# Kernel tuning notes

Hardware: AMD Instinct MI355X
Metric: run time of the kernel (lower is better)

The kernel has to match this reference:

```python
import jax, jax.numpy as jnp
import numpy as np
import math

N = 100000      # nodes
E = 1600000     # edges
D = 128         # embedding_size
H = 8           # num_heads
Dh = D // H     # head dim
F = 4 * D       # ffn hidden


def _layer_norm(x, g, b, eps=1e-5):
    mu = jnp.mean(x, axis=-1, keepdims=True)
    var = jnp.mean((x - mu) ** 2, axis=-1, keepdims=True)
    return (x - mu) * jax.lax.rsqrt(var + eps) * g + b


def setup_inputs() -> dict:
    key = jax.random.key(0)
    ks = jax.random.split(key, 12)
    s = 1.0 / math.sqrt(D)
    sf = 1.0 / math.sqrt(F)
    return {
        "feat": jax.random.normal(ks[0], (N, D), dtype=jnp.float32),
        "src": jax.random.randint(ks[1], (E,), 0, N, dtype=jnp.int32),
        "dst": jax.random.randint(ks[2], (E,), 0, N, dtype=jnp.int32),
        "Wq": jax.random.normal(ks[3], (D, D), dtype=jnp.float32) * s,
        "bq": jnp.zeros((D,), jnp.float32),
        "Wk": jax.random.normal(ks[4], (D, D), dtype=jnp.float32) * s,
        "bk": jnp.zeros((D,), jnp.float32),
        "Wv": jax.random.normal(ks[5], (D, D), dtype=jnp.float32) * s,
        "bv": jnp.zeros((D,), jnp.float32),
        "ln_g": jnp.ones((D,), jnp.float32),
        "ln_b": jnp.zeros((D,), jnp.float32),
        "W1": jax.random.normal(ks[6], (D, F), dtype=jnp.float32) * s,
        "b1": jnp.zeros((F,), jnp.float32),
        "alpha": jnp.full((F,), 0.25, jnp.float32),   # PReLU per-channel
        "W2": jax.random.normal(ks[7], (F, D), dtype=jnp.float32) * sf,
        "b2": jnp.zeros((D,), jnp.float32),
    }


def reference(feat, src, dst, Wq, bq, Wk, bk, Wv, bv, ln_g, ln_b, W1, b1, alpha, W2, b2):
    feat_c = jax.lax.stop_gradient(feat)  # feat_c = feat.detach()
    q = (feat @ Wq + bq).reshape(N, H, Dh)
    k = (feat_c @ Wk + bk).reshape(N, H, Dh)
    v = (feat_c @ Wv + bv).reshape(N, H, Dh)

    # u_dot_v: score per edge = <k[src], q[dst]> per head, scaled by sqrt(embedding_size)
    e = jnp.einsum('ehd,ehd->eh', k[src], q[dst]) / math.sqrt(D)  # [E, H]

    # edge_softmax over incoming edges of each destination node
    emax = jax.ops.segment_max(e, dst, num_segments=N)            # [N, H]
    ex = jnp.exp(e - emax[dst])                                   # [E, H]
    denom = jax.ops.segment_sum(ex, dst, num_segments=N)          # [N, H]
    a = ex / denom[dst]                                           # [E, H]

    # u_mul_e + sum: weighted scatter-aggregation into dst nodes
    m = v[src] * a[:, :, None]                                    # [E, H, Dh]
    rst = jax.ops.segment_sum(m, dst, num_segments=N)             # [N, H, Dh]
    rst = rst.reshape(N, D) + feat
    rst = _layer_norm(rst, ln_g, ln_b)

    # out_proj: Linear -> PReLU -> Linear (dropouts are identity at p=0)
    h = rst @ W1 + b1
    h = jnp.where(h > 0, h, alpha * h)
    ffn = h @ W2 + b2
    return _layer_norm(rst + ffn, ln_g, ln_b)  # original reuses ln1
```

## Files before the change

kernel.cpp:

```cpp
#include <hip/hip_runtime.h>
#include <hip/hip_bf16.h>

#define D 128
#define H 8
#define DH 16
#define FF 512
#define NBK 512
#define CHUNK 8192

typedef __hip_bfloat16 bf16;
typedef __attribute__((ext_vector_type(8))) short short8v;
typedef __attribute__((ext_vector_type(4))) float f32x4;

#define MFMA16(a, b, c) __builtin_amdgcn_mfma_f32_16x16x32_bf16((a), (b), (c), 0, 0, 0)

__device__ __forceinline__ unsigned short bfbits(float x) {
    bf16 h = __float2bfloat16(x);
    unsigned short s;
    __builtin_memcpy(&s, &h, 2);
    return s;
}

__device__ __forceinline__ void dec8(uint4 u, float* f) {
    f[0] = __uint_as_float(u.x << 16); f[1] = __uint_as_float(u.x & 0xffff0000u);
    f[2] = __uint_as_float(u.y << 16); f[3] = __uint_as_float(u.y & 0xffff0000u);
    f[4] = __uint_as_float(u.z << 16); f[5] = __uint_as_float(u.z & 0xffff0000u);
    f[6] = __uint_as_float(u.w << 16); f[7] = __uint_as_float(u.w & 0xffff0000u);
}

__global__ __launch_bounds__(256) void wsplit_pack(
    const float* __restrict__ W, unsigned short* __restrict__ Th,
    unsigned short* __restrict__ Tl, int K, int logC)
{
    int i = blockIdx.x * 256 + threadIdx.x;
    int total = K << logC;
    if (i >= total) return;
    int k = i >> logC;
    int n = i & ((1 << logC) - 1);
    float x = W[i];
    unsigned short hb = bfbits(x);
    float hf = __uint_as_float((unsigned)hb << 16);
    unsigned short lb = bfbits(x - hf);
    int NT = 1 << (logC - 4);
    int tile = (k >> 5) * NT + (n >> 4);
    int lane = ((k >> 3) & 3) * 16 + (n & 15);
    int idx = tile * 512 + lane * 8 + (k & 7);
    Th[idx] = hb;
    Tl[idx] = lb;
}

#define QXS 136

__global__ __launch_bounds__(256, 2) void qkv_mfma(
    const float* __restrict__ feat,
    const unsigned short* __restrict__ WTh, const unsigned short* __restrict__ WTl,
    const float* __restrict__ bq, const float* __restrict__ bk, const float* __restrict__ bv,
    bf16* __restrict__ q, bf16* __restrict__ k, bf16* __restrict__ v,
    int N)
{
    __shared__ unsigned short Xh[32 * QXS];
    __shared__ unsigned short Xl[32 * QXS];

    const int tid = threadIdx.x;
    const int n0 = blockIdx.x * 32;

    #pragma unroll
    for (int it = 0; it < 4; it++) {
        int idx = tid + it * 256;
        int row = idx >> 5;
        int part = idx & 31;
        float4 f = make_float4(0.f, 0.f, 0.f, 0.f);
        if (n0 + row < N) f = *(const float4*)(feat + (size_t)(n0 + row) * D + part * 4);
        const float xv[4] = {f.x, f.y, f.z, f.w};
        unsigned short hb[4], lb[4];
        #pragma unroll
        for (int j = 0; j < 4; j++) {
            hb[j] = bfbits(xv[j]);
            float hf = __uint_as_float((unsigned)hb[j] << 16);
            lb[j] = bfbits(xv[j] - hf);
        }
        uint2 ph, pl;
        ph.x = (unsigned)hb[0] | ((unsigned)hb[1] << 16);
        ph.y = (unsigned)hb[2] | ((unsigned)hb[3] << 16);
        pl.x = (unsigned)lb[0] | ((unsigned)lb[1] << 16);
        pl.y = (unsigned)lb[2] | ((unsigned)lb[3] << 16);
        *(uint2*)&Xh[row * QXS + part * 4] = ph;
        *(uint2*)&Xl[row * QXS + part * 4] = pl;
    }
    __syncthreads();

    const int w = tid >> 6, l = tid & 63;
    const int lr = l & 15;
    const int lg = l >> 4;

    f32x4 acc[2][6];
    const f32x4 zero4 = {0.f, 0.f, 0.f, 0.f};
    #pragma unroll
    for (int rt = 0; rt < 2; rt++)
        #pragma unroll
        for (int ct = 0; ct < 6; ct++) acc[rt][ct] = zero4;

    auto ldb = [&](int u, short8v* bh3, short8v* bl3) {
        const int ks = u >> 1, cb = (u & 1) * 3;
        #pragma unroll
        for (int j = 0; j < 3; j++) {
            const int g = w * 6 + cb + j;
            const size_t off = (size_t)(g >> 3) * 16384 +
                               (size_t)((ks * 8 + (g & 7)) * 512 + l * 8);
            bh3[j] = *(const short8v*)&WTh[off];
            bl3[j] = *(const short8v*)&WTl[off];
        }
    };

    short8v pbh[3][3], pbl[3][3];
    ldb(0, pbh[0], pbl[0]);
    ldb(1, pbh[1], pbl[1]);
    short8v ah0, ah1, al0, al1;

    #pragma unroll
    for (int u = 0; u < 8; u++) {
        if (u + 2 < 8) ldb(u + 2, pbh[(u + 2) % 3], pbl[(u + 2) % 3]);
        if ((u & 1) == 0) {
            const int k0 = (u >> 1) * 32;
            ah0 = *(const short8v*)&Xh[lr * QXS + k0 + lg * 8];
            ah1 = *(const short8v*)&Xh[(16 + lr) * QXS + k0 + lg * 8];
            al0 = *(const short8v*)&Xl[lr * QXS + k0 + lg * 8];
            al1 = *(const short8v*)&Xl[(16 + lr) * QXS + k0 + lg * 8];
        }
        const int cb = (u & 1) * 3;
        const short8v* bh = pbh[u % 3];
        const short8v* bl = pbl[u % 3];
        #pragma unroll
        for (int j = 0; j < 3; j++) acc[0][cb + j] = MFMA16(ah0, bh[j], acc[0][cb + j]);
        #pragma unroll
        for (int j = 0; j < 3; j++) acc[1][cb + j] = MFMA16(ah1, bh[j], acc[1][cb + j]);
        #pragma unroll
        for (int j = 0; j < 3; j++) acc[0][cb + j] = MFMA16(ah0, bl[j], acc[0][cb + j]);
        #pragma unroll
        for (int j = 0; j < 3; j++) acc[1][cb + j] = MFMA16(ah1, bl[j], acc[1][cb + j]);
        #pragma unroll
        for (int j = 0; j < 3; j++) acc[0][cb + j] = MFMA16(al0, bh[j], acc[0][cb + j]);
        #pragma unroll
        for (int j = 0; j < 3; j++) acc[1][cb + j] = MFMA16(al1, bh[j], acc[1][cb + j]);
    }

    #pragma unroll
    for (int ct = 0; ct < 6; ct++) {
        const int cbase = w * 96 + ct * 16;
        const int which = cbase >> 7;
        const int colin = (cbase & 127) + lr;
        const float* bias = which == 0 ? bq : (which == 1 ? bk : bv);
        bf16* outp       = which == 0 ? q  : (which == 1 ? k  : v);
        const float bb = bias[colin];
        #pragma unroll
        for (int rt = 0; rt < 2; rt++) {
            #pragma unroll
            for (int i = 0; i < 4; i++) {
                int row = n0 + rt * 16 + lg * 4 + i;
                if (row < N)
                    outp[(size_t)row * D + colin] = __float2bfloat16(acc[rt][ct][i] + bb);
            }
        }
    }
}

__global__ __launch_bounds__(256) void bucket_hist(
    const int* __restrict__ dst, int* __restrict__ bcnt, int E)
{
    __shared__ int bh[NBK];
    for (int j = threadIdx.x; j < NBK; j += 256) bh[j] = 0;
    __syncthreads();
    for (int i = blockIdx.x * 256 + threadIdx.x; i < E; i += gridDim.x * 256)
        atomicAdd(&bh[dst[i] >> 8], 1);
    __syncthreads();
    for (int j = threadIdx.x; j < NBK; j += 256)
        if (bh[j]) atomicAdd(&bcnt[j], bh[j]);
}

__global__ __launch_bounds__(256) void bucket_scan(
    const int* __restrict__ bcnt, int* __restrict__ bofsb, int* __restrict__ gcur)
{
    __shared__ int sA[NBK], sB[NBK];
    const int t = threadIdx.x;
    for (int j = t; j < NBK; j += 256) sA[j] = bcnt[j];
    __syncthreads();
    bool pb = false;
    for (int off = 1; off < NBK; off <<= 1) {
        const int* in = pb ? sB : sA;
        int* o        = pb ? sA : sB;
        for (int j = t; j < NBK; j += 256)
            o[j] = in[j] + (j >= off ? in[j - off] : 0);
        __syncthreads();
        pb = !pb;
    }
    const int* inc = pb ? sB : sA;
    for (int j = t; j < NBK; j += 256) {
        int ex = inc[j] - bcnt[j];
        bofsb[j] = ex;
        gcur[j]  = ex;
    }
}

__global__ __launch_bounds__(256) void binA(
    const int* __restrict__ src, const int* __restrict__ dst,
    int* __restrict__ gcur, unsigned* __restrict__ bpack, int E)
{
    __shared__ int hist[NBK], runc[NBK], gof[NBK];
    const int t = threadIdx.x;
    const int e0 = blockIdx.x * CHUNK;
    const int cnt = min(CHUNK, E - e0);

    for (int j = t; j < NBK; j += 256) { hist[j] = 0; runc[j] = 0; }
    __syncthreads();

    for (int i = t; i < cnt; i += 256)
        atomicAdd(&hist[dst[e0 + i] >> 8], 1);
    __syncthreads();

    for (int j = t; j < NBK; j += 256)
        if (hist[j] > 0) gof[j] = atomicAdd(&gcur[j], hist[j]);
    __syncthreads();

    for (int i = t; i < cnt; i += 256) {
        int d = dst[e0 + i];
        int s = src[e0 + i];
        int b = d >> 8;
        int r = atomicAdd(&runc[b], 1);
        bpack[gof[b] + r] = ((unsigned)(d & 255) << 24) | (unsigned)s;
    }
}

__global__ __launch_bounds__(256) void deg_binned(
    const unsigned* __restrict__ bpack, const int* __restrict__ bofsb,
    const int* __restrict__ bcnt, int* __restrict__ deg, int N)
{
    __shared__ int dc[256];
    const int t = threadIdx.x;
    const int b = blockIdx.x;
    dc[t] = 0;
    __syncthreads();
    const int bstart = bofsb[b], cnt = bcnt[b];
    for (int i = t; i < cnt; i += 256)
        atomicAdd(&dc[bpack[bstart + i] >> 24], 1);
    __syncthreads();
    const int node = b * 256 + t;
    if (node < N) deg[node] = dc[t];
}

__global__ __launch_bounds__(256) void binB(
    const unsigned* __restrict__ bpack, const int* __restrict__ bofsb,
    const int* __restrict__ bcnt, const int* __restrict__ row_off,
    int* __restrict__ csr, int N)
{
    __shared__ int curl[256];
    const int t = threadIdx.x;
    const int b = blockIdx.x;
    const int base = b * 256;
    curl[t] = (base + t < N) ? row_off[base + t] : 0;
    __syncthreads();
    const int bstart = bofsb[b], cnt = bcnt[b];
    for (int i = t; i < cnt; i += 256) {
        unsigned p = bpack[bstart + i];
        int pos = atomicAdd(&curl[p >> 24], 1);
        csr[pos] = (int)(p & 0xFFFFFFu);
    }
}

__global__ __launch_bounds__(256) void scan_bsum(
    const int* __restrict__ deg, int* __restrict__ bsum, int N)
{
    int base = blockIdx.x * 1024;
    int t = threadIdx.x;
    int s = 0;
    #pragma unroll
    for (int j = 0; j < 4; j++) {
        int i = base + t + 256 * j;
        if (i < N) s += deg[i];
    }
    #pragma unroll
    for (int o = 1; o < 64; o <<= 1) s += __shfl_xor(s, o);
    __shared__ int ws[4];
    if ((t & 63) == 0) ws[t >> 6] = s;
    __syncthreads();
    if (t == 0) bsum[blockIdx.x] = ws[0] + ws[1] + ws[2] + ws[3];
}

__global__ void scan_bofs(const int* __restrict__ bsum, int* __restrict__ bofs, int nb)
{
    if (threadIdx.x == 0) {
        int run = 0;
        for (int i = 0; i < nb; i++) { bofs[i] = run; run += bsum[i]; }
    }
}

__global__ __launch_bounds__(256) void scan_write(
    const int* __restrict__ deg, const int* __restrict__ bofs,
    int* __restrict__ row_off, int N)
{
    int t = threadIdx.x;
    int base = blockIdx.x * 1024 + t * 4;
    int d[4]; int tot = 0;
    #pragma unroll
    for (int j = 0; j < 4; j++) {
        int i = base + j;
        d[j] = (i < N) ? deg[i] : 0;
        tot += d[j];
    }
    int incl = tot;
    int lane = t & 63;
    #pragma unroll
    for (int o = 1; o < 64; o <<= 1) {
        int nv = __shfl_up(incl, o);
        if (lane >= o) incl += nv;
    }
    __shared__ int ws[4];
    if (lane == 63) ws[t >> 6] = incl;
    __syncthreads();
    int w = t >> 6;
    int woff = 0;
    #pragma unroll
    for (int kk = 0; kk < 4; kk++) if (kk < w) woff += ws[kk];
    int run = bofs[blockIdx.x] + woff + incl - tot;
    #pragma unroll
    for (int j = 0; j < 4; j++) {
        int i = base + j;
        if (i < N) row_off[i] = run;
        run += d[j];
    }
}

__global__ __launch_bounds__(64) void node_agg(
    const bf16* __restrict__ kb, const bf16* __restrict__ qb, const bf16* __restrict__ vb,
    const int* __restrict__ csr, const int* __restrict__ row_off, const int* __restrict__ deg,
    const float* __restrict__ feat, const float* __restrict__ g, const float* __restrict__ b,
    bf16* __restrict__ rst_ln, int N)
{
    __shared__ float qs[128];
    const int l = threadIdx.x;
    const int n = blockIdx.x;
    if (n >= N) return;

    unsigned qu = *(const unsigned*)(qb + (size_t)n * D + 2 * l);
    qs[2 * l]     = __uint_as_float(qu << 16);
    qs[2 * l + 1] = __uint_as_float(qu & 0xffff0000u);

    const int rs = row_off[n], dn = deg[n];
    const int el = l >> 3, h = l & 7, ha = l >> 3;

    float m = -3.0e38f, lsum = 0.f, acc0 = 0.f, acc1 = 0.f;

    if (dn > 0) {
        int sn = csr[rs + (el < dn ? el : 0)];
        const uint4* kp0 = (const uint4*)(kb + (size_t)sn * D + h * DH);
        uint4 k0 = kp0[0], k1 = kp0[1];

        for (int base = 0; base < dn; base += 8) {
            int sn_n = 0;
            uint4 kn0, kn1;
            const bool more = base + 8 < dn;
            if (more) {
                int ei = base + 8 + el;
                sn_n = csr[rs + (ei < dn ? ei : 0)];
                const uint4* kpn = (const uint4*)(kb + (size_t)sn_n * D + h * DH);
                kn0 = kpn[0]; kn1 = kpn[1];
            }

            const bool valid = base + el < dn;
            float kf[16];
            dec8(k0, kf); dec8(k1, kf + 8);
            const float* qp = &qs[h * DH];
            float s = 0.f;
            #pragma unroll
            for (int i = 0; i < 16; i++) s += kf[i] * qp[i];
            s *= 0.08838834764831845f;
            if (!valid) s = -3.0e38f;

            float cmax = s;
            cmax = fmaxf(cmax, __shfl_xor(cmax, 8));
            cmax = fmaxf(cmax, __shfl_xor(cmax, 16));
            cmax = fmaxf(cmax, __shfl_xor(cmax, 32));
            float m_new = fmaxf(m, cmax);
            float alphaH = __expf(m - m_new);
            float wgt = __expf(s - m_new);
            float wsum = wgt;
            wsum += __shfl_xor(wsum, 8);
            wsum += __shfl_xor(wsum, 16);
            wsum += __shfl_xor(wsum, 32);
            lsum = lsum * alphaH + wsum;
            m = m_new;

            float alphaA = __shfl(alphaH, ha);

            float na0 = 0.f, na1 = 0.f;
            #pragma unroll
            for (int e = 0; e < 8; e++) {
                int sne = __shfl(sn, e * 8);
                unsigned vu = *(const unsigned*)(vb + (size_t)sne * D + 2 * l);
                float wv = __shfl(wgt, e * 8 + ha);
                na0 += wv * __uint_as_float(vu << 16);
                na1 += wv * __uint_as_float(vu & 0xffff0000u);
            }
            acc0 = acc0 * alphaA + na0;
            acc1 = acc1 * alphaA + na1;

            if (more) { sn = sn_n; k0 = kn0; k1 = kn1; }
        }
    }

    float den = __shfl(lsum, ha);
    float v0 = (den > 0.f) ? acc0 / den : 0.f;
    float v1 = (den > 0.f) ? acc1 / den : 0.f;

    float2 fv = *(const float2*)(feat + (size_t)n * D + 2 * l);
    v0 += fv.x; v1 += fv.y;

    float s1 = v0 + v1, s2 = v0 * v0 + v1 * v1;
    #pragma unroll
    for (int o = 1; o < 64; o <<= 1) {
        s1 += __shfl_xor(s1, o);
        s2 += __shfl_xor(s2, o);
    }
    float mu = s1 * (1.f / 128.f);
    float var = s2 * (1.f / 128.f) - mu * mu;
    float rsq = rsqrtf(var + 1e-5f);
    float y0 = (v0 - mu) * rsq * g[2 * l]     + b[2 * l];
    float y1 = (v1 - mu) * rsq * g[2 * l + 1] + b[2 * l + 1];
    unsigned pk = (unsigned)bfbits(y0) | ((unsigned)bfbits(y1) << 16);
    *(unsigned*)(rst_ln + (size_t)n * D + 2 * l) = pk;
}

#define BM 32
#define XS 136
#define HS 520
#define YS 132

__global__ __launch_bounds__(256, 2) void ffn_mfma(
    const bf16* __restrict__ rst_ln,
    const unsigned short* __restrict__ W1Th, const unsigned short* __restrict__ W1Tl,
    const float* __restrict__ b1, const float* __restrict__ alpha,
    const unsigned short* __restrict__ W2Th, const unsigned short* __restrict__ W2Tl,
    const float* __restrict__ b2,
    const float* __restrict__ g, const float* __restrict__ bln,
    float* __restrict__ out, int N)
{
    __shared__ unsigned short Xs[BM * XS];
    __shared__ unsigned short HhBuf[BM * HS];
    __shared__ unsigned short Hl[BM * HS];

    const int tid = threadIdx.x;
    const int n0 = blockIdx.x * BM;

    #pragma unroll
    for (int it = 0; it < 2; it++) {
        int idx = tid + it * 256;
        int row = idx >> 4;
        int part = idx & 15;
        uint4 u = make_uint4(0u, 0u, 0u, 0u);
        if (n0 + row < N) u = *(const uint4*)(rst_ln + (size_t)(n0 + row) * D + part * 8);
        *(uint4*)&Xs[row * XS + part * 8] = u;
    }
    __syncthreads();

    const int w = tid >> 6, l = tid & 63;
    const int lr = l & 15;
    const int lg = l >> 4;

    const int colbase = w * 128;
    f32x4 acc1[2][8];
    const f32x4 zero4 = {0.f, 0.f, 0.f, 0.f};
    #pragma unroll
    for (int rt = 0; rt < 2; rt++)
        #pragma unroll
        for (int ct = 0; ct < 8; ct++) acc1[rt][ct] = zero4;

    auto ldb1 = [&](int u, short8v* bh4, short8v* bl4) {
        const int ks = u >> 1, cb = (u & 1) * 4;
        #pragma unroll
        for (int j = 0; j < 4; j++) {
            const size_t off = (size_t)((ks * 32 + w * 8 + cb + j) * 512 + l * 8);
            bh4[j] = *(const short8v*)&W1Th[off];
            bl4[j] = *(const short8v*)&W1Tl[off];
        }
    };

    {
        short8v pbh[3][4], pbl[3][4];
        ldb1(0, pbh[0], pbl[0]);
        ldb1(1, pbh[1], pbl[1]);
        short8v a0, a1;
        #pragma unroll
        for (int u = 0; u < 8; u++) {
            if (u + 2 < 8) ldb1(u + 2, pbh[(u + 2) % 3], pbl[(u + 2) % 3]);
            if ((u & 1) == 0) {
                const int k0 = (u >> 1) * 32;
                a0 = *(const short8v*)&Xs[lr * XS + k0 + lg * 8];
                a1 = *(const short8v*)&Xs[(16 + lr) * XS + k0 + lg * 8];
            }
            const int cb = (u & 1) * 4;
            const short8v* bh = pbh[u % 3];
            const short8v* bl = pbl[u % 3];
            #pragma unroll
            for (int j = 0; j < 4; j++) acc1[0][cb + j] = MFMA16(a0, bh[j], acc1[0][cb + j]);
            #pragma unroll
            for (int j = 0; j < 4; j++) acc1[1][cb + j] = MFMA16(a1, bh[j], acc1[1][cb + j]);
            #pragma unroll
            for (int j = 0; j < 4; j++) acc1[0][cb + j] = MFMA16(a0, bl[j], acc1[0][cb + j]);
            #pragma unroll
            for (int j = 0; j < 4; j++) acc1[1][cb + j] = MFMA16(a1, bl[j], acc1[1][cb + j]);
        }
    }

    #pragma unroll
    for (int ct = 0; ct < 8; ct++) {
        const int col = colbase + ct * 16 + lr;
        const float bb = b1[col];
        const float aa = alpha[col];
        #pragma unroll
        for (int rt = 0; rt < 2; rt++) {
            #pragma unroll
            for (int i = 0; i < 4; i++) {
                const int row = rt * 16 + lg * 4 + i;
                float hv = acc1[rt][ct][i] + bb;
                hv = hv > 0.f ? hv : aa * hv;
                unsigned short hb = bfbits(hv);
                float hf = __uint_as_float((unsigned)hb << 16);
                unsigned short lb = bfbits(hv - hf);
                HhBuf[row * HS + col] = hb;
                Hl[row * HS + col]    = lb;
            }
        }
    }
    __syncthreads();

    const int ob = w * 32;
    f32x4 acc2[2][2];
    #pragma unroll
    for (int rt = 0; rt < 2; rt++)
        #pragma unroll
        for (int ct = 0; ct < 2; ct++) acc2[rt][ct] = zero4;

    auto ldb2 = [&](int ks, short8v* bh2, short8v* bl2) {
        #pragma unroll
        for (int ct = 0; ct < 2; ct++) {
            const size_t off = (size_t)((ks * 8 + w * 2 + ct) * 512 + l * 8);
            bh2[ct] = *(const short8v*)&W2Th[off];
            bl2[ct] = *(const short8v*)&W2Tl[off];
        }
    };

    {
        short8v p2h[4][2], p2l[4][2];
        #pragma unroll
        for (int s = 0; s < 3; s++) ldb2(s, p2h[s], p2l[s]);
        #pragma unroll
        for (int ks = 0; ks < 16; ks++) {
            const int slot = ks & 3;
            if (ks + 3 < 16) ldb2(ks + 3, p2h[(ks + 3) & 3], p2l[(ks + 3) & 3]);
            const int k0 = ks * 32;
            short8v ah0 = *(const short8v*)&HhBuf[lr * HS + k0 + lg * 8];
            short8v ah1 = *(const short8v*)&HhBuf[(16 + lr) * HS + k0 + lg * 8];
            short8v al0 = *(const short8v*)&Hl[lr * HS + k0 + lg * 8];
            short8v al1 = *(const short8v*)&Hl[(16 + lr) * HS + k0 + lg * 8];
            const short8v* bh = p2h[slot];
            const short8v* bl = p2l[slot];
            acc2[0][0] = MFMA16(ah0, bh[0], acc2[0][0]);
            acc2[0][1] = MFMA16(ah0, bh[1], acc2[0][1]);
            acc2[1][0] = MFMA16(ah1, bh[0], acc2[1][0]);
            acc2[1][1] = MFMA16(ah1, bh[1], acc2[1][1]);
            acc2[0][0] = MFMA16(ah0, bl[0], acc2[0][0]);
            acc2[0][1] = MFMA16(ah0, bl[1], acc2[0][1]);
            acc2[1][0] = MFMA16(ah1, bl[0], acc2[1][0]);
            acc2[1][1] = MFMA16(ah1, bl[1], acc2[1][1]);
            acc2[0][0] = MFMA16(al0, bh[0], acc2[0][0]);
            acc2[0][1] = MFMA16(al0, bh[1], acc2[0][1]);
            acc2[1][0] = MFMA16(al1, bh[0], acc2[1][0]);
            acc2[1][1] = MFMA16(al1, bh[1], acc2[1][1]);
        }
    }
    __syncthreads();

    float* Yb = (float*)HhBuf;
    #pragma unroll
    for (int ct = 0; ct < 2; ct++) {
        const int col = ob + ct * 16 + lr;
        const float bb = b2[col];
        #pragma unroll
        for (int rt = 0; rt < 2; rt++) {
            #pragma unroll
            for (int i = 0; i < 4; i++) {
                const int row = rt * 16 + lg * 4 + i;
                float xr = __uint_as_float((unsigned)Xs[row * XS + col] << 16);
                Yb[row * YS + col] = acc2[rt][ct][i] + bb + xr;
            }
        }
    }
    __syncthreads();

    {
        const int row = tid >> 3;
        const int sub = tid & 7;
        const int c0 = sub * 16;
        const float* Yr = Yb + row * YS + c0;
        f32x4 v0 = *(const f32x4*)(Yr + 0);
        f32x4 v1 = *(const f32x4*)(Yr + 4);
        f32x4 v2 = *(const f32x4*)(Yr + 8);
        f32x4 v3 = *(const f32x4*)(Yr + 12);
        float s1 = 0.f, s2 = 0.f;
        #pragma unroll
        for (int c = 0; c < 4; c++) {
            s1 += v0[c] + v1[c] + v2[c] + v3[c];
            s2 += v0[c] * v0[c] + v1[c] * v1[c] + v2[c] * v2[c] + v3[c] * v3[c];
        }
        #pragma unroll
        for (int o = 1; o < 8; o <<= 1) {
            s1 += __shfl_xor(s1, o);
            s2 += __shfl_xor(s2, o);
        }
        float mu = s1 * (1.f / 128.f);
        float var = s2 * (1.f / 128.f) - mu * mu;
        float rs = rsqrtf(var + 1e-5f);
        const int gr = n0 + row;
        if (gr < N) {
            float* op = out + (size_t)gr * D + c0;
            f32x4 g0 = *(const f32x4*)(g + c0 + 0),  g1 = *(const f32x4*)(g + c0 + 4);
            f32x4 g2 = *(const f32x4*)(g + c0 + 8),  g3 = *(const f32x4*)(g + c0 + 12);
            f32x4 b0 = *(const f32x4*)(bln + c0 + 0), b1v = *(const f32x4*)(bln + c0 + 4);
            f32x4 b2v = *(const f32x4*)(bln + c0 + 8), b3 = *(const f32x4*)(bln + c0 + 12);
            *(f32x4*)(op + 0)  = (v0 - mu) * rs * g0 + b0;
            *(f32x4*)(op + 4)  = (v1 - mu) * rs * g1 + b1v;
            *(f32x4*)(op + 8)  = (v2 - mu) * rs * g2 + b2v;
            *(f32x4*)(op + 12) = (v3 - mu) * rs * g3 + b3;
        }
    }
}

extern "C" void kernel_launch(void* const* d_in, const int* in_sizes, int n_in,
                              void* d_out, int out_size, void* d_ws, size_t ws_size,
                              hipStream_t stream) {
    const float* feat = (const float*)d_in[0];
    const int*   src  = (const int*)d_in[1];
    const int*   dst  = (const int*)d_in[2];
    const float* Wq   = (const float*)d_in[3];
    const float* bq   = (const float*)d_in[4];
    const float* Wk   = (const float*)d_in[5];
    const float* bk   = (const float*)d_in[6];
    const float* Wv   = (const float*)d_in[7];
    const float* bv   = (const float*)d_in[8];
    const float* ln_g = (const float*)d_in[9];
    const float* ln_b = (const float*)d_in[10];
    const float* W1   = (const float*)d_in[11];
    const float* b1   = (const float*)d_in[12];
    const float* alp  = (const float*)d_in[13];
    const float* W2   = (const float*)d_in[14];
    const float* b2   = (const float*)d_in[15];
    float* out = (float*)d_out;

    const int N = in_sizes[0] / D;
    const int E = in_sizes[1];
    const int nb = (N + 1023) / 1024;
    const int nbk = (N + 255) >> 8;

    char* p = (char*)d_ws;
    auto take = [&](size_t bytes) { char* r = p; p += (bytes + 255) & ~(size_t)255; return r; };
    bf16* qb    = (bf16*)take((size_t)N * D * 2);
    bf16* kb    = (bf16*)take((size_t)N * D * 2);
    bf16* vb    = (bf16*)take((size_t)N * D * 2);
    bf16* rstln = (bf16*)take((size_t)N * D * 2);
    int*  degb  = (int*)take((size_t)N * 4);
    int*  rowof = (int*)take((size_t)N * 4);
    int*  csr   = (int*)take((size_t)E * 4);
    unsigned* bpack = (unsigned*)take((size_t)E * 4);
    int*  bsum  = (int*)take((size_t)nb * 4);
    int*  bofs  = (int*)take((size_t)nb * 4);
    int*  bcnt  = (int*)take((size_t)NBK * 4);
    int*  bofsb = (int*)take((size_t)NBK * 4);
    int*  gcur  = (int*)take((size_t)NBK * 4);
    unsigned short* w1th = (unsigned short*)take((size_t)D * FF * 2);
    unsigned short* w1tl = (unsigned short*)take((size_t)D * FF * 2);
    unsigned short* w2th = (unsigned short*)take((size_t)D * FF * 2);
    unsigned short* w2tl = (unsigned short*)take((size_t)D * FF * 2);
    unsigned short* wqkvh = (unsigned short*)take((size_t)3 * D * D * 2);
    unsigned short* wqkvl = (unsigned short*)take((size_t)3 * D * D * 2);

    wsplit_pack<<<(D * FF + 255) / 256, 256, 0, stream>>>(W1, w1th, w1tl, D, 9);
    wsplit_pack<<<(D * FF + 255) / 256, 256, 0, stream>>>(W2, w2th, w2tl, FF, 7);
    wsplit_pack<<<(D * D + 255) / 256, 256, 0, stream>>>(Wq, wqkvh,             wqkvl,             D, 7);
    wsplit_pack<<<(D * D + 255) / 256, 256, 0, stream>>>(Wk, wqkvh + D * D,     wqkvl + D * D,     D, 7);
    wsplit_pack<<<(D * D + 255) / 256, 256, 0, stream>>>(Wv, wqkvh + 2 * D * D, wqkvl + 2 * D * D, D, 7);

    qkv_mfma<<<(N + 31) / 32, 256, 0, stream>>>(
        feat, wqkvh, wqkvl, bq, bk, bv, qb, kb, vb, N);

    hipMemsetAsync(bcnt, 0, (size_t)NBK * 4, stream);
    bucket_hist<<<256, 256, 0, stream>>>(dst, bcnt, E);
    bucket_scan<<<1, 256, 0, stream>>>(bcnt, bofsb, gcur);
    binA<<<(E + CHUNK - 1) / CHUNK, 256, 0, stream>>>(src, dst, gcur, bpack, E);
    deg_binned<<<nbk, 256, 0, stream>>>(bpack, bofsb, bcnt, degb, N);
    scan_bsum<<<nb, 256, 0, stream>>>(degb, bsum, N);
    scan_bofs<<<1, 64, 0, stream>>>(bsum, bofs, nb);
    scan_write<<<nb, 256, 0, stream>>>(degb, bofs, rowof, N);
    binB<<<nbk, 256, 0, stream>>>(bpack, bofsb, bcnt, rowof, csr, N);

    node_agg<<<N, 64, 0, stream>>>(
        kb, qb, vb, csr, rowof, degb, feat, ln_g, ln_b, rstln, N);

    ffn_mfma<<<(N + BM - 1) / BM, 256, 0, stream>>>(
        rstln, w1th, w1tl, b1, alp, w2th, w2tl, b2, ln_g, ln_b, out, N);
}
```

Measured before the change: 492.9 us.

## Cut LDS and register use in QKV and FFN kernels to raise occupancy

Raises the launch-bounds occupancy targets for the QKV and FFN MFMA kernels and drops the software-pipelined weight prefetch rings, which lowers register pressure. The FFN kernel no longer stages the input tile in LDS: A fragments and the residual come straight from global memory. The hidden activation's hi and lo bf16 halves now share one LDS buffer in two passes, with the lo half rebuilt from the fp32 accumulators that stay in registers. This roughly halves LDS per block, at the cost of an extra pass and barrier, reloading W2Th, and more exposed global load latency.

```diff
diff --git a/kernel.cpp b/kernel.cpp
--- a/kernel.cpp
+++ b/kernel.cpp
@@ -51,7 +51,7 @@
 
 #define QXS 136
 
-__global__ __launch_bounds__(256, 2) void qkv_mfma(
+__global__ __launch_bounds__(256, 4) void qkv_mfma(
     const float* __restrict__ feat,
     const unsigned short* __restrict__ WTh, const unsigned short* __restrict__ WTl,
     const float* __restrict__ bq, const float* __restrict__ bk, const float* __restrict__ bv,
@@ -100,8 +100,12 @@
         #pragma unroll
         for (int ct = 0; ct < 6; ct++) acc[rt][ct] = zero4;
 
-    auto ldb = [&](int u, short8v* bh3, short8v* bl3) {
+    short8v ah0, ah1, al0, al1;
+
+    #pragma unroll
+    for (int u = 0; u < 8; u++) {
         const int ks = u >> 1, cb = (u & 1) * 3;
+        short8v bh3[3], bl3[3];
         #pragma unroll
         for (int j = 0; j < 3; j++) {
             const int g = w * 6 + cb + j;
@@ -110,38 +114,25 @@
             bh3[j] = *(const short8v*)&WTh[off];
             bl3[j] = *(const short8v*)&WTl[off];
         }
-    };
-
-    short8v pbh[3][3], pbl[3][3];
-    ldb(0, pbh[0], pbl[0]);
-    ldb(1, pbh[1], pbl[1]);
-    short8v ah0, ah1, al0, al1;
-
-    #pragma unroll
-    for (int u = 0; u < 8; u++) {
-        if (u + 2 < 8) ldb(u + 2, pbh[(u + 2) % 3], pbl[(u + 2) % 3]);
         if ((u & 1) == 0) {
-            const int k0 = (u >> 1) * 32;
+            const int k0 = ks * 32;
             ah0 = *(const short8v*)&Xh[lr * QXS + k0 + lg * 8];
             ah1 = *(const short8v*)&Xh[(16 + lr) * QXS + k0 + lg * 8];
             al0 = *(const short8v*)&Xl[lr * QXS + k0 + lg * 8];
             al1 = *(const short8v*)&Xl[(16 + lr) * QXS + k0 + lg * 8];
         }
-        const int cb = (u & 1) * 3;
-        const short8v* bh = pbh[u % 3];
-        const short8v* bl = pbl[u % 3];
-        #pragma unroll
-        for (int j = 0; j < 3; j++) acc[0][cb + j] = MFMA16(ah0, bh[j], acc[0][cb + j]);
-        #pragma unroll
-        for (int j = 0; j < 3; j++) acc[1][cb + j] = MFMA16(ah1, bh[j], acc[1][cb + j]);
-        #pragma unroll
-        for (int j = 0; j < 3; j++) acc[0][cb + j] = MFMA16(ah0, bl[j], acc[0][cb + j]);
-        #pragma unroll
-        for (int j = 0; j < 3; j++) acc[1][cb + j] = MFMA16(ah1, bl[j], acc[1][cb + j]);
-        #pragma unroll
-        for (int j = 0; j < 3; j++) acc[0][cb + j] = MFMA16(al0, bh[j], acc[0][cb + j]);
-        #pragma unroll
-        for (int j = 0; j < 3; j++) acc[1][cb + j] = MFMA16(al1, bh[j], acc[1][cb + j]);
+        #pragma unroll
+        for (int j = 0; j < 3; j++) acc[0][cb + j] = MFMA16(ah0, bh3[j], acc[0][cb + j]);
+        #pragma unroll
+        for (int j = 0; j < 3; j++) acc[1][cb + j] = MFMA16(ah1, bh3[j], acc[1][cb + j]);
+        #pragma unroll
+        for (int j = 0; j < 3; j++) acc[0][cb + j] = MFMA16(ah0, bl3[j], acc[0][cb + j]);
+        #pragma unroll
+        for (int j = 0; j < 3; j++) acc[1][cb + j] = MFMA16(ah1, bl3[j], acc[1][cb + j]);
+        #pragma unroll
+        for (int j = 0; j < 3; j++) acc[0][cb + j] = MFMA16(al0, bh3[j], acc[0][cb + j]);
+        #pragma unroll
+        for (int j = 0; j < 3; j++) acc[1][cb + j] = MFMA16(al1, bh3[j], acc[1][cb + j]);
     }
 
     #pragma unroll
@@ -430,11 +421,10 @@
 }
 
 #define BM 32
-#define XS 136
 #define HS 520
 #define YS 132
 
-__global__ __launch_bounds__(256, 2) void ffn_mfma(
+__global__ __launch_bounds__(256, 3) void ffn_mfma(
     const bf16* __restrict__ rst_ln,
     const unsigned short* __restrict__ W1Th, const unsigned short* __restrict__ W1Tl,
     const float* __restrict__ b1, const float* __restrict__ alpha,
@@ -443,24 +433,10 @@
     const float* __restrict__ g, const float* __restrict__ bln,
     float* __restrict__ out, int N)
 {
-    __shared__ unsigned short Xs[BM * XS];
-    __shared__ unsigned short HhBuf[BM * HS];
-    __shared__ unsigned short Hl[BM * HS];
+    __shared__ unsigned short Hb[BM * HS];
 
     const int tid = threadIdx.x;
     const int n0 = blockIdx.x * BM;
-
-    #pragma unroll
-    for (int it = 0; it < 2; it++) {
-        int idx = tid + it * 256;
-        int row = idx >> 4;
-        int part = idx & 15;
-        uint4 u = make_uint4(0u, 0u, 0u, 0u);
-        if (n0 + row < N) u = *(const uint4*)(rst_ln + (size_t)(n0 + row) * D + part * 8);
-        *(uint4*)&Xs[row * XS + part * 8] = u;
-    }
-    __syncthreads();
-
     const int w = tid >> 6, l = tid & 63;
     const int lr = l & 15;
     const int lg = l >> 4;
@@ -473,40 +449,38 @@
         #pragma unroll
         for (int ct = 0; ct < 8; ct++) acc1[rt][ct] = zero4;
 
-    auto ldb1 = [&](int u, short8v* bh4, short8v* bl4) {
-        const int ks = u >> 1, cb = (u & 1) * 4;
-        #pragma unroll
-        for (int j = 0; j < 4; j++) {
-            const size_t off = (size_t)((ks * 32 + w * 8 + cb + j) * 512 + l * 8);
-            bh4[j] = *(const short8v*)&W1Th[off];
-            bl4[j] = *(const short8v*)&W1Tl[off];
-        }
+    auto lda = [&](int mt, int k0) {
+        short8v a = {0, 0, 0, 0, 0, 0, 0, 0};
+        const int row = n0 + mt * 16 + lr;
+        if (row < N)
+            a = *(const short8v*)((const unsigned short*)rst_ln + (size_t)row * D + k0 + lg * 8);
+        return a;
     };
 
     {
-        short8v pbh[3][4], pbl[3][4];
-        ldb1(0, pbh[0], pbl[0]);
-        ldb1(1, pbh[1], pbl[1]);
-        short8v a0, a1;
+        short8v a0 = {0,0,0,0,0,0,0,0}, a1 = {0,0,0,0,0,0,0,0};
         #pragma unroll
         for (int u = 0; u < 8; u++) {
-            if (u + 2 < 8) ldb1(u + 2, pbh[(u + 2) % 3], pbl[(u + 2) % 3]);
+            const int ks = u >> 1, cb = (u & 1) * 4;
+            short8v bh4[4], bl4[4];
+            #pragma unroll
+            for (int j = 0; j < 4; j++) {
+                const size_t off = (size_t)((ks * 32 + w * 8 + cb + j) * 512 + l * 8);
+                bh4[j] = *(const short8v*)&W1Th[off];
+                bl4[j] = *(const short8v*)&W1Tl[off];
+            }
             if ((u & 1) == 0) {
-                const int k0 = (u >> 1) * 32;
-                a0 = *(const short8v*)&Xs[lr * XS + k0 + lg * 8];
-                a1 = *(const short8v*)&Xs[(16 + lr) * XS + k0 + lg * 8];
+                a0 = lda(0, ks * 32);
+                a1 = lda(1, ks * 32);
             }
-            const int cb = (u & 1) * 4;
-            const short8v* bh = pbh[u % 3];
-            const short8v* bl = pbl[u % 3];
-            #pragma unroll
-            for (int j = 0; j < 4; j++) acc1[0][cb + j] = MFMA16(a0, bh[j], acc1[0][cb + j]);
-            #pragma unroll
-            for (int j = 0; j < 4; j++) acc1[1][cb + j] = MFMA16(a1, bh[j], acc1[1][cb + j]);
-            #pragma unroll
-            for (int j = 0; j < 4; j++) acc1[0][cb + j] = MFMA16(a0, bl[j], acc1[0][cb + j]);
-            #pragma unroll
-            for (int j = 0; j < 4; j++) acc1[1][cb + j] = MFMA16(a1, bl[j], acc1[1][cb + j]);
+            #pragma unroll
+            for (int j = 0; j < 4; j++) acc1[0][cb + j] = MFMA16(a0, bh4[j], acc1[0][cb + j]);
+            #pragma unroll
+            for (int j = 0; j < 4; j++) acc1[1][cb + j] = MFMA16(a1, bh4[j], acc1[1][cb + j]);
+            #pragma unroll
+            for (int j = 0; j < 4; j++) acc1[0][cb + j] = MFMA16(a0, bl4[j], acc1[0][cb + j]);
+            #pragma unroll
+            for (int j = 0; j < 4; j++) acc1[1][cb + j] = MFMA16(a1, bl4[j], acc1[1][cb + j]);
         }
     }
 
@@ -522,11 +496,7 @@
                 const int row = rt * 16 + lg * 4 + i;
                 float hv = acc1[rt][ct][i] + bb;
                 hv = hv > 0.f ? hv : aa * hv;
-                unsigned short hb = bfbits(hv);
-                float hf = __uint_as_float((unsigned)hb << 16);
-                unsigned short lb = bfbits(hv - hf);
-                HhBuf[row * HS + col] = hb;
-                Hl[row * HS + col]    = lb;
+                Hb[row * HS + col] = bfbits(hv);
             }
         }
     }
@@ -539,47 +509,68 @@
         #pragma unroll
         for (int ct = 0; ct < 2; ct++) acc2[rt][ct] = zero4;
 
-    auto ldb2 = [&](int ks, short8v* bh2, short8v* bl2) {
+    #pragma unroll
+    for (int ks = 0; ks < 16; ks++) {
+        const int k0 = ks * 32;
+        short8v bh2[2], bl2[2];
         #pragma unroll
         for (int ct = 0; ct < 2; ct++) {
             const size_t off = (size_t)((ks * 8 + w * 2 + ct) * 512 + l * 8);
             bh2[ct] = *(const short8v*)&W2Th[off];
             bl2[ct] = *(const short8v*)&W2Tl[off];
         }
-    };
-
-    {
-        short8v p2h[4][2], p2l[4][2];
-        #pragma unroll
-        for (int s = 0; s < 3; s++) ldb2(s, p2h[s], p2l[s]);
-        #pragma unroll
-        for (int ks = 0; ks < 16; ks++) {
-            const int slot = ks & 3;
-            if (ks + 3 < 16) ldb2(ks + 3, p2h[(ks + 3) & 3], p2l[(ks + 3) & 3]);
-            const int k0 = ks * 32;
-            short8v ah0 = *(const short8v*)&HhBuf[lr * HS + k0 + lg * 8];
-            short8v ah1 = *(const short8v*)&HhBuf[(16 + lr) * HS + k0 + lg * 8];
-            short8v al0 = *(const short8v*)&Hl[lr * HS + k0 + lg * 8];
-            short8v al1 = *(const short8v*)&Hl[(16 + lr) * HS + k0 + lg * 8];
-            const short8v* bh = p2h[slot];
-            const short8v* bl = p2l[slot];
-            acc2[0][0] = MFMA16(ah0, bh[0], acc2[0][0]);
-            acc2[0][1] = MFMA16(ah0, bh[1], acc2[0][1]);
-            acc2[1][0] = MFMA16(ah1, bh[0], acc2[1][0]);
-            acc2[1][1] = MFMA16(ah1, bh[1], acc2[1][1]);
-            acc2[0][0] = MFMA16(ah0, bl[0], acc2[0][0]);
-            acc2[0][1] = MFMA16(ah0, bl[1], acc2[0][1]);
-            acc2[1][0] = MFMA16(ah1, bl[0], acc2[1][0]);
-            acc2[1][1] = MFMA16(ah1, bl[1], acc2[1][1]);
-            acc2[0][0] = MFMA16(al0, bh[0], acc2[0][0]);
-            acc2[0][1] = MFMA16(al0, bh[1], acc2[0][1]);
-            acc2[1][0] = MFMA16(al1, bh[0], acc2[1][0]);
-            acc2[1][1] = MFMA16(al1, bh[1], acc2[1][1]);
-        }
-    }
-    __syncthreads();
-
-    float* Yb = (float*)HhBuf;
+        short8v ah0 = *(const short8v*)&Hb[lr * HS + k0 + lg * 8];
+        short8v ah1 = *(const short8v*)&Hb[(16 + lr) * HS + k0 + lg * 8];
+        acc2[0][0] = MFMA16(ah0, bh2[0], acc2[0][0]);
+        acc2[0][1] = MFMA16(ah0, bh2[1], acc2[0][1]);
+        acc2[1][0] = MFMA16(ah1, bh2[0], acc2[1][0]);
+        acc2[1][1] = MFMA16(ah1, bh2[1], acc2[1][1]);
+        acc2[0][0] = MFMA16(ah0, bl2[0], acc2[0][0]);
+        acc2[0][1] = MFMA16(ah0, bl2[1], acc2[0][1]);
+        acc2[1][0] = MFMA16(ah1, bl2[0], acc2[1][0]);
+        acc2[1][1] = MFMA16(ah1, bl2[1], acc2[1][1]);
+    }
+    __syncthreads();
+
+    #pragma unroll
+    for (int ct = 0; ct < 8; ct++) {
+        const int col = colbase + ct * 16 + lr;
+        const float bb = b1[col];
+        const float aa = alpha[col];
+        #pragma unroll
+        for (int rt = 0; rt < 2; rt++) {
+            #pragma unroll
+            for (int i = 0; i < 4; i++) {
+                const int row = rt * 16 + lg * 4 + i;
+                float hv = acc1[rt][ct][i] + bb;
+                hv = hv > 0.f ? hv : aa * hv;
+                unsigned short hbb = bfbits(hv);
+                float hf = __uint_as_float((unsigned)hbb << 16);
+                Hb[row * HS + col] = bfbits(hv - hf);
+            }
+        }
+    }
+    __syncthreads();
+
+    #pragma unroll
+    for (int ks = 0; ks < 16; ks++) {
+        const int k0 = ks * 32;
+        short8v bh2[2];
+        #pragma unroll
+        for (int ct = 0; ct < 2; ct++) {
+            const size_t off = (size_t)((ks * 8 + w * 2 + ct) * 512 + l * 8);
+            bh2[ct] = *(const short8v*)&W2Th[off];
+        }
+        short8v al0 = *(const short8v*)&Hb[lr * HS + k0 + lg * 8];
+        short8v al1 = *(const short8v*)&Hb[(16 + lr) * HS + k0 + lg * 8];
+        acc2[0][0] = MFMA16(al0, bh2[0], acc2[0][0]);
+        acc2[0][1] = MFMA16(al0, bh2[1], acc2[0][1]);
+        acc2[1][0] = MFMA16(al1, bh2[0], acc2[1][0]);
+        acc2[1][1] = MFMA16(al1, bh2[1], acc2[1][1]);
+    }
+    __syncthreads();
+
+    float* Yb = (float*)Hb;
     #pragma unroll
     for (int ct = 0; ct < 2; ct++) {
         const int col = ob + ct * 16 + lr;
@@ -589,7 +580,12 @@
             #pragma unroll
             for (int i = 0; i < 4; i++) {
                 const int row = rt * 16 + lg * 4 + i;
-                float xr = __uint_as_float((unsigned)Xs[row * XS + col] << 16);
+                const int gr = n0 + row;
+                float xr = 0.f;
+                if (gr < N) {
+                    unsigned short xb = *((const unsigned short*)rst_ln + (size_t)gr * D + col);
+                    xr = __uint_as_float((unsigned)xb << 16);
+                }
                 Yb[row * YS + col] = acc2[rt][ct][i] + bb + xr;
             }
         }
```

After: 515.7 us. 1.05x slower.

## Fuse CSR degree, scan and scatter into one kernel; merge weight packing launches

Applied to the files above, without the earlier changes.

Bucket-local degree counts are now prefix-scanned inside each bucket block and offset by the bucket's global start, which replaces the separate degree, three-kernel global scan and binB passes with a single kernel. The five weight-splitting launches and the memset of the bucket counts are merged into one 2D-grid kernel. This cuts about eight launches and one pass over the binned edge array. It relies on the bucket offsets already matching the node-ordered CSR layout. For the smaller weights most blocks in the merged grid exit immediately.

```diff
diff --git a/kernel.cpp b/kernel.cpp
--- a/kernel.cpp
+++ b/kernel.cpp
@@ -28,10 +28,30 @@
     f[6] = __uint_as_float(u.w << 16); f[7] = __uint_as_float(u.w & 0xffff0000u);
 }
 
-__global__ __launch_bounds__(256) void wsplit_pack(
-    const float* __restrict__ W, unsigned short* __restrict__ Th,
-    unsigned short* __restrict__ Tl, int K, int logC)
-{
+__global__ __launch_bounds__(256) void wsplit_all(
+    const float* __restrict__ W1, const float* __restrict__ W2,
+    const float* __restrict__ Wq, const float* __restrict__ Wk, const float* __restrict__ Wv,
+    unsigned short* __restrict__ w1th, unsigned short* __restrict__ w1tl,
+    unsigned short* __restrict__ w2th, unsigned short* __restrict__ w2tl,
+    unsigned short* __restrict__ wqh,  unsigned short* __restrict__ wql,
+    int* __restrict__ bcnt)
+{
+    const int y = blockIdx.y;
+    const float* W;
+    unsigned short *Th, *Tl;
+    int K, logC;
+    if (y == 0)      { W = W1; Th = w1th; Tl = w1tl; K = 128; logC = 9; }
+    else if (y == 1) { W = W2; Th = w2th; Tl = w2tl; K = 512; logC = 7; }
+    else {
+        const int m = y - 2;
+        W  = m == 0 ? Wq : (m == 1 ? Wk : Wv);
+        Th = wqh + m * (D * D);
+        Tl = wql + m * (D * D);
+        K = 128; logC = 7;
+    }
+    if (y == 0 && blockIdx.x == 0)
+        for (int j = threadIdx.x; j < NBK; j += 256) bcnt[j] = 0;
+
     int i = blockIdx.x * 256 + threadIdx.x;
     int total = K << logC;
     if (i >= total) return;
@@ -230,102 +250,49 @@
     }
 }
 
-__global__ __launch_bounds__(256) void deg_binned(
+__global__ __launch_bounds__(256) void binB_fused(
     const unsigned* __restrict__ bpack, const int* __restrict__ bofsb,
-    const int* __restrict__ bcnt, int* __restrict__ deg, int N)
+    const int* __restrict__ bcnt,
+    int* __restrict__ deg, int* __restrict__ row_off,
+    int* __restrict__ csr, int N)
 {
     __shared__ int dc[256];
+    __shared__ int curl[256];
+    __shared__ int wsum[4];
     const int t = threadIdx.x;
     const int b = blockIdx.x;
+    const int bstart = bofsb[b], cnt = bcnt[b];
+
     dc[t] = 0;
     __syncthreads();
-    const int bstart = bofsb[b], cnt = bcnt[b];
     for (int i = t; i < cnt; i += 256)
         atomicAdd(&dc[bpack[bstart + i] >> 24], 1);
     __syncthreads();
+
+    const int myDeg = dc[t];
+    int incl = myDeg;
+    const int lane = t & 63;
+    #pragma unroll
+    for (int o = 1; o < 64; o <<= 1) {
+        int nv = __shfl_up(incl, o);
+        if (lane >= o) incl += nv;
+    }
+    if (lane == 63) wsum[t >> 6] = incl;
+    __syncthreads();
+    int woff = 0;
+    #pragma unroll
+    for (int kk = 0; kk < 4; kk++) if (kk < (t >> 6)) woff += wsum[kk];
+    const int ex = bstart + woff + incl - myDeg;
+
+    curl[t] = ex;
     const int node = b * 256 + t;
-    if (node < N) deg[node] = dc[t];
-}
-
-__global__ __launch_bounds__(256) void binB(
-    const unsigned* __restrict__ bpack, const int* __restrict__ bofsb,
-    const int* __restrict__ bcnt, const int* __restrict__ row_off,
-    int* __restrict__ csr, int N)
-{
-    __shared__ int curl[256];
-    const int t = threadIdx.x;
-    const int b = blockIdx.x;
-    const int base = b * 256;
-    curl[t] = (base + t < N) ? row_off[base + t] : 0;
-    __syncthreads();
-    const int bstart = bofsb[b], cnt = bcnt[b];
+    if (node < N) { deg[node] = myDeg; row_off[node] = ex; }
+    __syncthreads();
+
     for (int i = t; i < cnt; i += 256) {
         unsigned p = bpack[bstart + i];
         int pos = atomicAdd(&curl[p >> 24], 1);
         csr[pos] = (int)(p & 0xFFFFFFu);
-    }
-}
-
-__global__ __launch_bounds__(256) void scan_bsum(
-    const int* __restrict__ deg, int* __restrict__ bsum, int N)
-{
-    int base = blockIdx.x * 1024;
-    int t = threadIdx.x;
-    int s = 0;
-    #pragma unroll
-    for (int j = 0; j < 4; j++) {
-        int i = base + t + 256 * j;
-        if (i < N) s += deg[i];
-    }
-    #pragma unroll
-    for (int o = 1; o < 64; o <<= 1) s += __shfl_xor(s, o);
-    __shared__ int ws[4];
-    if ((t & 63) == 0) ws[t >> 6] = s;
-    __syncthreads();
-    if (t == 0) bsum[blockIdx.x] = ws[0] + ws[1] + ws[2] + ws[3];
-}
-
-__global__ void scan_bofs(const int* __restrict__ bsum, int* __restrict__ bofs, int nb)
-{
-    if (threadIdx.x == 0) {
-        int run = 0;
-        for (int i = 0; i < nb; i++) { bofs[i] = run; run += bsum[i]; }
-    }
-}
-
-__global__ __launch_bounds__(256) void scan_write(
-    const int* __restrict__ deg, const int* __restrict__ bofs,
-    int* __restrict__ row_off, int N)
-{
-    int t = threadIdx.x;
-    int base = blockIdx.x * 1024 + t * 4;
-    int d[4]; int tot = 0;
-    #pragma unroll
-    for (int j = 0; j < 4; j++) {
-        int i = base + j;
-        d[j] = (i < N) ? deg[i] : 0;
-        tot += d[j];
-    }
-    int incl = tot;
-    int lane = t & 63;
-    #pragma unroll
-    for (int o = 1; o < 64; o <<= 1) {
-        int nv = __shfl_up(incl, o);
-        if (lane >= o) incl += nv;
-    }
-    __shared__ int ws[4];
-    if (lane == 63) ws[t >> 6] = incl;
-    __syncthreads();
-    int w = t >> 6;
-    int woff = 0;
-    #pragma unroll
-    for (int kk = 0; kk < 4; kk++) if (kk < w) woff += ws[kk];
-    int run = bofs[blockIdx.x] + woff + incl - tot;
-    #pragma unroll
-    for (int j = 0; j < 4; j++) {
-        int i = base + j;
-        if (i < N) row_off[i] = run;
-        run += d[j];
     }
 }
 
@@ -657,7 +624,6 @@
 
     const int N = in_sizes[0] / D;
     const int E = in_sizes[1];
-    const int nb = (N + 1023) / 1024;
     const int nbk = (N + 255) >> 8;
 
     char* p = (char*)d_ws;
@@ -670,8 +636,6 @@
     int*  rowof = (int*)take((size_t)N * 4);
     int*  csr   = (int*)take((size_t)E * 4);
     unsigned* bpack = (unsigned*)take((size_t)E * 4);
-    int*  bsum  = (int*)take((size_t)nb * 4);
-    int*  bofs  = (int*)take((size_t)nb * 4);
     int*  bcnt  = (int*)take((size_t)NBK * 4);
     int*  bofsb = (int*)take((size_t)NBK * 4);
     int*  gcur  = (int*)take((size_t)NBK * 4);
@@ -682,24 +646,16 @@
     unsigned short* wqkvh = (unsigned short*)take((size_t)3 * D * D * 2);
     unsigned short* wqkvl = (unsigned short*)take((size_t)3 * D * D * 2);
 
-    wsplit_pack<<<(D * FF + 255) / 256, 256, 0, stream>>>(W1, w1th, w1tl, D, 9);
-    wsplit_pack<<<(D * FF + 255) / 256, 256, 0, stream>>>(W2, w2th, w2tl, FF, 7);
-    wsplit_pack<<<(D * D + 255) / 256, 256, 0, stream>>>(Wq, wqkvh,             wqkvl,             D, 7);
-    wsplit_pack<<<(D * D + 255) / 256, 256, 0, stream>>>(Wk, wqkvh + D * D,     wqkvl + D * D,     D, 7);
-    wsplit_pack<<<(D * D + 255) / 256, 256, 0, stream>>>(Wv, wqkvh + 2 * D * D, wqkvl + 2 * D * D, D, 7);
+    wsplit_all<<<dim3((D * FF + 255) / 256, 5), 256, 0, stream>>>(
+        W1, W2, Wq, Wk, Wv, w1th, w1tl, w2th, w2tl, wqkvh, wqkvl, bcnt);
 
     qkv_mfma<<<(N + 31) / 32, 256, 0, stream>>>(
         feat, wqkvh, wqkvl, bq, bk, bv, qb, kb, vb, N);
 
-    hipMemsetAsync(bcnt, 0, (size_t)NBK * 4, stream);
     bucket_hist<<<256, 256, 0, stream>>>(dst, bcnt, E);
     bucket_scan<<<1, 256, 0, stream>>>(bcnt, bofsb, gcur);
     binA<<<(E + CHUNK - 1) / CHUNK, 256, 0, stream>>>(src, dst, gcur, bpack, E);
-    deg_binned<<<nbk, 256, 0, stream>>>(bpack, bofsb, bcnt, degb, N);
-    scan_bsum<<<nb, 256, 0, stream>>>(degb, bsum, N);
-    scan_bofs<<<1, 64, 0, stream>>>(bsum, bofs, nb);
-    scan_write<<<nb, 256, 0, stream>>>(degb, bofs, rowof, N);
-    binB<<<nbk, 256, 0, stream>>>(bpack, bofsb, bcnt, rowof, csr, N);
+    binB_fused<<<nbk, 256, 0, stream>>>(bpack, bofsb, bcnt, degb, rowof, csr, N);
 
     node_agg<<<N, 64, 0, stream>>>(
         kb, qb, vb, csr, rowof, degb, feat, ln_g, ln_b, rstln, N);
```

Result: faster. 468.5 us (-5.0%).
